# Optimization experiments

Hardware: AMD Instinct MI355X
Metric: run time of the kernel (lower is better)

Reference implementation:

```python
import jax, jax.numpy as jnp
import numpy as np

CROP = 512
GRID = 8
NBINS = 256
CLIP_LIMIT = 0.8


def _clahe(x):
    # x: [B, C, H, W] in [0, 1], H and W divisible by GRID
    B, C, H, W = x.shape
    th, tw = H // GRID, W // GRID
    tp = th * tw  # pixels per tile
    # bin index of each pixel (256 uniform bins over [0, 1])
    bins = jnp.clip((x * NBINS).astype(jnp.int32), 0, NBINS - 1)
    # per-tile histograms: [B*C*GRID*GRID, tp] -> scatter-add into 256 bins
    tiles = bins.reshape(B, C, GRID, th, GRID, tw).transpose(0, 1, 2, 4, 3, 5).reshape(-1, tp)
    hist = jax.vmap(lambda b: jnp.zeros((NBINS,), jnp.float32).at[b].add(1.0))(tiles)
    # clip histogram and redistribute excess uniformly
    clip_val = max(CLIP_LIMIT * tp / NBINS, 1.0)
    clipped = jnp.minimum(hist, clip_val)
    excess = (hist - clipped).sum(-1, keepdims=True)
    hist = clipped + excess / NBINS
    # CDF -> LUT per tile, values in [0, 255]
    lut = jnp.clip(jnp.cumsum(hist, -1) * ((NBINS - 1.0) / tp), 0.0, NBINS - 1.0)
    luts = lut.reshape(B, C, GRID, GRID, NBINS)
    # bilinear interpolation between the 4 nearest tile LUTs
    ty = (jnp.arange(H, dtype=jnp.float32) + 0.5) / th - 0.5
    tx = (jnp.arange(W, dtype=jnp.float32) + 0.5) / tw - 0.5
    y0f, x0f = jnp.floor(ty), jnp.floor(tx)
    fy = (ty - y0f)[None, None, :, None]
    fx = (tx - x0f)[None, None, None, :]
    y0 = jnp.clip(y0f, 0, GRID - 1).astype(jnp.int32)
    y1 = jnp.clip(y0f + 1, 0, GRID - 1).astype(jnp.int32)
    x0 = jnp.clip(x0f, 0, GRID - 1).astype(jnp.int32)
    x1 = jnp.clip(x0f + 1, 0, GRID - 1).astype(jnp.int32)
    bi = jnp.arange(B)[:, None, None, None]
    ci = jnp.arange(C)[None, :, None, None]
    Y0 = y0[None, None, :, None]
    Y1 = y1[None, None, :, None]
    X0 = x0[None, None, None, :]
    X1 = x1[None, None, None, :]
    v00 = luts[bi, ci, Y0, X0, bins]
    v01 = luts[bi, ci, Y0, X1, bins]
    v10 = luts[bi, ci, Y1, X0, bins]
    v11 = luts[bi, ci, Y1, X1, bins]
    top = (1.0 - fx) * v00 + fx * v01
    bot = (1.0 - fx) * v10 + fx * v11
    return ((1.0 - fy) * top + fy * bot) / (NBINS - 1.0)


def _augment(x, hflip, vflip, offy, offx, apply_clahe):
    # per-sample horizontal / vertical flips
    x = jnp.where(hflip[:, None, None, None].astype(bool), x[..., ::-1], x)
    x = jnp.where(vflip[:, None, None, None].astype(bool), x[..., ::-1, :], x)
    # per-sample random 512x512 crop
    C = x.shape[1]
    crop = jax.vmap(
        lambda img, oy, ox: jax.lax.dynamic_slice(img, (0, oy, ox), (C, CROP, CROP))
    )(x, offy, offx)
    # RandomApply(CLAHE): compute for all samples, select per sample
    eq = _clahe(crop)
    return jnp.where(apply_clahe[:, None, None, None].astype(bool), eq, crop)


def setup_inputs() -> dict:
    key = jax.random.key(0)
    ks = jax.random.split(key, 6)
    B, C, H, W = 64, 1, 640, 640
    x = jax.random.uniform(ks[0], (B, C, H, W), dtype=jnp.float32)
    hflip = jax.random.randint(ks[1], (B,), 0, 2, dtype=jnp.int32)
    vflip = jax.random.randint(ks[2], (B,), 0, 2, dtype=jnp.int32)
    offy = jax.random.randint(ks[3], (B,), 0, H - CROP + 1, dtype=jnp.int32)
    offx = jax.random.randint(ks[4], (B,), 0, W - CROP + 1, dtype=jnp.int32)
    apply_clahe = jax.random.randint(ks[5], (B,), 0, 2, dtype=jnp.int32)
    return {"x": x, "hflip": hflip, "vflip": vflip, "offy": offy, "offx": offx, "apply_clahe": apply_clahe}


def reference(x, hflip, vflip, offy, offx, apply_clahe):
    return _augment(x, hflip, vflip, offy, offx, apply_clahe)
```

## Files before the change

### kernel.cpp

```cpp
#include <hip/hip_runtime.h>

#define IH 640
#define IW 640
#define CROPSZ 512
#define NGRID 8
#define TILE 64
#define NBINS 256
#define TP (TILE*TILE)
#define CLIPV 12.8f

typedef float fvec4 __attribute__((ext_vector_type(4)));

__global__ __launch_bounds__(256) void clahe_lut_kernel(
    const float* __restrict__ x,
    const int* __restrict__ hflip, const int* __restrict__ vflip,
    const int* __restrict__ offy,  const int* __restrict__ offx,
    const int* __restrict__ apply,
    float* __restrict__ luts)
{
    const int bt = blockIdx.x;
    const int b  = bt >> 6;
    if (!apply[b]) return;
    const int tile = bt & 63;
    const int tyi = tile >> 3, txi = tile & 7;

    const int oy = offy[b], ox = offx[b];
    const int by = tyi * TILE, bx = txi * TILE;
    const int sy = vflip[b] ? (IH - TILE - oy - by) : (oy + by);
    const int sx = hflip[b] ? (IW - TILE - ox - bx) : (ox + bx);

    __shared__ unsigned int hist[4][NBINS];
    const int t    = threadIdx.x;
    const int lane = t & 63;
    const int wid  = t >> 6;
    #pragma unroll
    for (int w = 0; w < 4; ++w) hist[w][t] = 0u;
    __syncthreads();

    const float* __restrict__ xb = x + (size_t)b * (IH * IW);

    #pragma unroll
    for (int k = 0; k < 4; ++k) {
        const int q    = t + k * 256;
        const int row  = q >> 4;
        const int col4 = (q & 15) << 2;
        const fvec4 v = *reinterpret_cast<const fvec4*>(
                             xb + (size_t)(sy + row) * IW + sx + col4);
        #pragma unroll
        for (int j = 0; j < 4; ++j) {
            int bin = (int)(v[j] * 256.0f);
            bin = bin < 0 ? 0 : (bin > 255 ? 255 : bin);
            atomicAdd(&hist[wid][bin], 1u);
        }
    }
    __syncthreads();

    const float h = (float)(hist[0][t] + hist[1][t] + hist[2][t] + hist[3][t]);
    const float clipped = fminf(h, CLIPV);
    float ex = h - clipped;

    #pragma unroll
    for (int off = 32; off > 0; off >>= 1) ex += __shfl_down(ex, off, 64);
    __shared__ float wsum[4];
    if (lane == 0) wsum[wid] = ex;
    __syncthreads();
    const float excess = wsum[0] + wsum[1] + wsum[2] + wsum[3];

    const float hv = clipped + excess * (1.0f / (float)NBINS);

    float s = hv;
    #pragma unroll
    for (int off = 1; off < 64; off <<= 1) {
        const float n = __shfl_up(s, off, 64);
        if (lane >= off) s += n;
    }
    __shared__ float wtot[4];
    if (lane == 63) wtot[wid] = s;
    __syncthreads();
    float prefix = 0.0f;
    for (int w = 0; w < wid; ++w) prefix += wtot[w];
    s += prefix;

    float lut = s * (255.0f / (float)TP);
    lut = fminf(fmaxf(lut, 0.0f), 255.0f);
    luts[(size_t)bt * NBINS + t] = lut;
}

__global__ __launch_bounds__(256) void augment_out_kernel(
    const float* __restrict__ x,
    const int* __restrict__ hflip, const int* __restrict__ vflip,
    const int* __restrict__ offy,  const int* __restrict__ offx,
    const int* __restrict__ apply,
    const float* __restrict__ luts,
    float* __restrict__ out)
{
    const int bid = blockIdx.x;
    const int b   = bid >> 8;
    const int blk = bid & 255;
    const int cb  = blk & 7;
    const int rb  = blk >> 3;

    const int t  = threadIdx.x;
    const int tc = t & 15;
    const int r  = t >> 4;

    const int y   = rb * 16 + r;
    const int col = cb * 64 + tc * 4;

    const int hf = hflip[b], vf = vflip[b];
    const int oy = offy[b],  ox = offx[b];
    const int ap = apply[b];

    const int iy = vf ? (IH - 1 - oy - y) : (oy + y);
    const float* __restrict__ row = x + (size_t)b * (IH * IW) + (size_t)iy * IW;

    fvec4 v;
    if (hf) {
        const fvec4 rr = *reinterpret_cast<const fvec4*>(row + (IW - 4 - ox - col));
        v = (fvec4){rr.w, rr.z, rr.y, rr.x};
    } else {
        v = *reinterpret_cast<const fvec4*>(row + ox + col);
    }

    fvec4 o;
    if (ap) {
        const int y0f = (int)floorf((rb * 16 + 0.5f) * (1.0f / TILE) - 0.5f);
        const int y0  = max(0, min(NGRID - 1, y0f));
        const int y1  = max(0, min(NGRID - 1, y0f + 1));

        __shared__ fvec4 lutq[2][NBINS];
        const float* __restrict__ lb = luts + (size_t)b * (64 * NBINS);
        #pragma unroll
        for (int h = 0; h < 2; ++h) {
            const int xl = max(0, min(NGRID - 1, cb - 1 + h));
            const int xr = max(0, min(NGRID - 1, cb + h));
            fvec4 q;
            q.x = lb[((y0 << 3) + xl) * NBINS + t];
            q.y = lb[((y0 << 3) + xr) * NBINS + t];
            q.z = lb[((y1 << 3) + xl) * NBINS + t];
            q.w = lb[((y1 << 3) + xr) * NBINS + t];
            lutq[h][t] = q;
        }
        __syncthreads();

        const float fy = (y + 0.5f) * (1.0f / TILE) - 0.5f - (float)y0f;
        const int   h  = tc >> 3;
        const float x0ff = (float)(cb - 1 + h);

        #pragma unroll
        for (int j = 0; j < 4; ++j) {
            const float fx = (col + j + 0.5f) * (1.0f / TILE) - 0.5f - x0ff;
            int bin = (int)(v[j] * 256.0f);
            bin = bin < 0 ? 0 : (bin > 255 ? 255 : bin);
            const fvec4 q = lutq[h][bin];
            const float top = (1.0f - fx) * q.x + fx * q.y;
            const float bot = (1.0f - fx) * q.z + fx * q.w;
            o[j] = ((1.0f - fy) * top + fy * bot) * (1.0f / 255.0f);
        }
    } else {
        o = v;
    }

    const size_t oidx = (size_t)b * (CROPSZ * CROPSZ / 4) + (size_t)y * (CROPSZ / 4) + (col >> 2);
    __builtin_nontemporal_store(o, reinterpret_cast<fvec4*>(out) + oidx);
}

extern "C" void kernel_launch(void* const* d_in, const int* in_sizes, int n_in,
                              void* d_out, int out_size, void* d_ws, size_t ws_size,
                              hipStream_t stream) {
    const float* x     = (const float*)d_in[0];
    const int*   hflip = (const int*)d_in[1];
    const int*   vflip = (const int*)d_in[2];
    const int*   offy  = (const int*)d_in[3];
    const int*   offx  = (const int*)d_in[4];
    const int*   apply = (const int*)d_in[5];
    float*       out   = (float*)d_out;
    float*       luts  = (float*)d_ws;

    hipLaunchKernelGGL(clahe_lut_kernel, dim3(64 * 64), dim3(256), 0, stream,
                       x, hflip, vflip, offy, offx, apply, luts);

    hipLaunchKernelGGL(augment_out_kernel, dim3(64 * 256), dim3(256), 0, stream,
                       x, hflip, vflip, offy, offx, apply, luts, out);
}
```

Before: 181.4 us.

## Enlarge output blocks to 64x64 tiles with four shared LUT quadrants

The output kernel now uses 1024-thread blocks that each cover a full 64x64 tile aligned to the CLAHE grid. It stages four interpolation LUT sets (one per quadrant) in shared memory, which cuts redundant LUT gathers from global memory per output pixel. Input loads in both kernels become nontemporal to avoid polluting the cache with streamed pixels. The larger blocks may reduce occupancy flexibility, and the shared-memory footprint is now 16KB per block.

```diff
diff --git a/kernel.cpp b/kernel.cpp
--- a/kernel.cpp
+++ b/kernel.cpp
@@ -44,8 +44,8 @@
         const int q    = t + k * 256;
         const int row  = q >> 4;
         const int col4 = (q & 15) << 2;
-        const fvec4 v = *reinterpret_cast<const fvec4*>(
-                             xb + (size_t)(sy + row) * IW + sx + col4);
+        const fvec4 v = __builtin_nontemporal_load(
+            reinterpret_cast<const fvec4*>(xb + (size_t)(sy + row) * IW + sx + col4));
         #pragma unroll
         for (int j = 0; j < 4; ++j) {
             int bin = (int)(v[j] * 256.0f);
@@ -86,7 +86,7 @@
     luts[(size_t)bt * NBINS + t] = lut;
 }
 
-__global__ __launch_bounds__(256) void augment_out_kernel(
+__global__ __launch_bounds__(1024) void augment_out_kernel(
     const float* __restrict__ x,
     const int* __restrict__ hflip, const int* __restrict__ vflip,
     const int* __restrict__ offy,  const int* __restrict__ offx,
@@ -94,18 +94,18 @@
     const float* __restrict__ luts,
     float* __restrict__ out)
 {
-    const int bid = blockIdx.x;
-    const int b   = bid >> 8;
-    const int blk = bid & 255;
-    const int cb  = blk & 7;
-    const int rb  = blk >> 3;
+    const int bid  = blockIdx.x;
+    const int b    = bid >> 6;
+    const int blk  = bid & 63;
+    const int cbig = blk & 7;
+    const int rbig = blk >> 3;
 
     const int t  = threadIdx.x;
     const int tc = t & 15;
     const int r  = t >> 4;
 
-    const int y   = rb * 16 + r;
-    const int col = cb * 64 + tc * 4;
+    const int y   = rbig * 64 + r;
+    const int col = cbig * 64 + tc * 4;
 
     const int hf = hflip[b], vf = vflip[b];
     const int oy = offy[b],  ox = offx[b];
@@ -116,43 +116,47 @@
 
     fvec4 v;
     if (hf) {
-        const fvec4 rr = *reinterpret_cast<const fvec4*>(row + (IW - 4 - ox - col));
+        const fvec4 rr = __builtin_nontemporal_load(
+            reinterpret_cast<const fvec4*>(row + (IW - 4 - ox - col)));
         v = (fvec4){rr.w, rr.z, rr.y, rr.x};
     } else {
-        v = *reinterpret_cast<const fvec4*>(row + ox + col);
+        v = __builtin_nontemporal_load(
+            reinterpret_cast<const fvec4*>(row + ox + col));
     }
 
     fvec4 o;
     if (ap) {
-        const int y0f = (int)floorf((rb * 16 + 0.5f) * (1.0f / TILE) - 0.5f);
-        const int y0  = max(0, min(NGRID - 1, y0f));
-        const int y1  = max(0, min(NGRID - 1, y0f + 1));
+        __shared__ fvec4 lutq[4][NBINS];
 
-        __shared__ fvec4 lutq[2][NBINS];
-        const float* __restrict__ lb = luts + (size_t)b * (64 * NBINS);
-        #pragma unroll
-        for (int h = 0; h < 2; ++h) {
-            const int xl = max(0, min(NGRID - 1, cb - 1 + h));
-            const int xr = max(0, min(NGRID - 1, cb + h));
+        {
+            const int tab = t >> 8;
+            const int bin = t & 255;
+            const int hy  = tab >> 1, hx = tab & 1;
+            const int y0  = max(0, min(NGRID - 1, rbig - 1 + hy));
+            const int y1  = max(0, min(NGRID - 1, rbig     + hy));
+            const int x0  = max(0, min(NGRID - 1, cbig - 1 + hx));
+            const int x1  = max(0, min(NGRID - 1, cbig     + hx));
+            const float* __restrict__ lb = luts + (size_t)b * (64 * NBINS);
             fvec4 q;
-            q.x = lb[((y0 << 3) + xl) * NBINS + t];
-            q.y = lb[((y0 << 3) + xr) * NBINS + t];
-            q.z = lb[((y1 << 3) + xl) * NBINS + t];
-            q.w = lb[((y1 << 3) + xr) * NBINS + t];
-            lutq[h][t] = q;
+            q.x = lb[((y0 << 3) + x0) * NBINS + bin];
+            q.y = lb[((y0 << 3) + x1) * NBINS + bin];
+            q.z = lb[((y1 << 3) + x0) * NBINS + bin];
+            q.w = lb[((y1 << 3) + x1) * NBINS + bin];
+            lutq[tab][bin] = q;
         }
         __syncthreads();
 
-        const float fy = (y + 0.5f) * (1.0f / TILE) - 0.5f - (float)y0f;
-        const int   h  = tc >> 3;
-        const float x0ff = (float)(cb - 1 + h);
+        const int hy  = r >> 5;
+        const int hx  = tc >> 3;
+        const int tab = hy * 2 + hx;
+        const float fy = (y + 0.5f) * (1.0f / TILE) - 0.5f - (float)(rbig - 1 + hy);
 
         #pragma unroll
         for (int j = 0; j < 4; ++j) {
-            const float fx = (col + j + 0.5f) * (1.0f / TILE) - 0.5f - x0ff;
+            const float fx = (col + j + 0.5f) * (1.0f / TILE) - 0.5f - (float)(cbig - 1 + hx);
             int bin = (int)(v[j] * 256.0f);
             bin = bin < 0 ? 0 : (bin > 255 ? 255 : bin);
-            const fvec4 q = lutq[h][bin];
+            const fvec4 q = lutq[tab][bin];
             const float top = (1.0f - fx) * q.x + fx * q.y;
             const float bot = (1.0f - fx) * q.z + fx * q.w;
             o[j] = ((1.0f - fy) * top + fy * bot) * (1.0f / 255.0f);
@@ -180,6 +184,6 @@
     hipLaunchKernelGGL(clahe_lut_kernel, dim3(64 * 64), dim3(256), 0, stream,
                        x, hflip, vflip, offy, offx, apply, luts);
 
-    hipLaunchKernelGGL(augment_out_kernel, dim3(64 * 256), dim3(256), 0, stream,
+    hipLaunchKernelGGL(augment_out_kernel, dim3(64 * 64), dim3(1024), 0, stream,
                        x, hflip, vflip, offy, offx, apply, luts, out);
 }
```

New measurement: 179.3 us. Within noise of the previous version (-1.1%).
